# Kernel tuning notes

Hardware: AMD Instinct MI355X
Metric: run time of the kernel (lower is better)

Reference implementation:

```python
import jax, jax.numpy as jnp
import numpy as np
import math

B, T, E, H = 8, 2048, 1024, 64  # batch, seq (== BLOCK_SIZE), emb_size, head_size


def setup_inputs() -> dict:
    key = jax.random.key(0)
    kx, kq, kk, kv = jax.random.split(key, 4)
    s = 1.0 / math.sqrt(E)
    return {
        "x": jax.random.normal(kx, (B, T, E), dtype=jnp.float32),
        "Wq": jax.random.uniform(kq, (H, E), dtype=jnp.float32, minval=-s, maxval=s),
        "Wk": jax.random.uniform(kk, (H, E), dtype=jnp.float32, minval=-s, maxval=s),
        "Wv": jax.random.uniform(kv, (H, E), dtype=jnp.float32, minval=-s, maxval=s),
        "should_mask": 1,
    }


def reference(x, Wq, Wk, Wv, should_mask):
    # Linear(E, H, bias=False): y = x @ W.T
    q = jnp.einsum("bte,he->bth", x, Wq)
    k = jnp.einsum("bte,he->bth", x, Wk)
    v = jnp.einsum("bte,he->bth", x, Wv)
    # NOTE: source multiplies by sqrt(head_size) (not the usual divide)
    affinity = jnp.einsum("bth,bsh->bts", q, k) * jnp.float32(math.sqrt(H))
    if should_mask:
        tril = jnp.tril(jnp.ones((T, T), dtype=bool))
        affinity = jnp.where(tril, affinity, jnp.float32(-jnp.inf))
    weight = jax.nn.softmax(affinity, axis=-1)
    # dropout omitted (eval mode) for determinism
    out = jnp.einsum("bts,bsh->bth", weight, v)
    return out
```

## Files before the change

### kernel.cpp

```cpp
#include <hip/hip_runtime.h>
#include <math.h>

#define NB 8
#define NT 2048
#define NE 1024
#define NH 64

typedef __attribute__((ext_vector_type(8))) short bh8;
typedef __attribute__((ext_vector_type(4))) float f4;

typedef unsigned short u16;

__device__ __forceinline__ u16 bf16rn(float f) {
    unsigned u = __float_as_uint(f);
    u += 0x7FFFu + ((u >> 16) & 1u);
    return (u16)(u >> 16);
}
__device__ __forceinline__ float bf16f(u16 h) {
    return __uint_as_float(((unsigned)h) << 16);
}

__global__ void wprep(const float* __restrict__ wq, const float* __restrict__ wk,
                      const float* __restrict__ wv,
                      u16* __restrict__ whi, u16* __restrict__ wlo)
{
    const int row = blockIdx.x;
    const int k0  = threadIdx.x * 4;
    const float* src = (row < 64)  ? (wq + (size_t)row * NE)
                     : (row < 128) ? (wk + (size_t)(row - 64) * NE)
                     :               (wv + (size_t)(row - 128) * NE);
    float4 v = *(const float4*)(src + k0);
    ushort4 h, l;
    h.x = bf16rn(v.x); l.x = bf16rn(v.x - bf16f(h.x));
    h.y = bf16rn(v.y); l.y = bf16rn(v.y - bf16f(h.y));
    h.z = bf16rn(v.z); l.z = bf16rn(v.z - bf16f(h.z));
    h.w = bf16rn(v.w); l.w = bf16rn(v.w - bf16f(h.w));
    *(ushort4*)(whi + (size_t)row * NE + k0) = h;
    *(ushort4*)(wlo + (size_t)row * NE + k0) = l;
}

__global__ __launch_bounds__(256, 2) void qkv_mfma(
    const float* __restrict__ x, const u16* __restrict__ whi_, const u16* __restrict__ wlo_,
    u16* __restrict__ qhi, u16* __restrict__ qlo,
    u16* __restrict__ khi, u16* __restrict__ klo, u16* __restrict__ vtp)
{
    __shared__ u16 xh[32][72], xl[32][72];
    __shared__ u16 wh[192][72], wl[192][72];

    const int tid  = threadIdx.x;
    const int wid  = tid >> 6;
    const int lane = tid & 63;
    const int t15  = lane & 15, t4 = lane >> 4;
    const int row0 = blockIdx.x * 32;

    const f4 fzero = {0.f, 0.f, 0.f, 0.f};
    f4 acc[2][3];
#pragma unroll
    for (int m = 0; m < 2; ++m)
#pragma unroll
        for (int n = 0; n < 3; ++n) acc[m][n] = fzero;

    for (int kt = 0; kt < NE; kt += 64) {
        __syncthreads();
#pragma unroll
        for (int it = 0; it < 2; ++it) {
            const int f = tid + it * 256;
            const int r = f >> 4, sg = f & 15;
            float4 v = *(const float4*)(x + (size_t)(row0 + r) * NE + kt + sg * 4);
            ushort4 h, l;
            h.x = bf16rn(v.x); l.x = bf16rn(v.x - bf16f(h.x));
            h.y = bf16rn(v.y); l.y = bf16rn(v.y - bf16f(h.y));
            h.z = bf16rn(v.z); l.z = bf16rn(v.z - bf16f(h.z));
            h.w = bf16rn(v.w); l.w = bf16rn(v.w - bf16f(h.w));
            *(ushort4*)&xh[r][sg * 4] = h;
            *(ushort4*)&xl[r][sg * 4] = l;
        }
#pragma unroll
        for (int it = 0; it < 6; ++it) {
            const int f = tid + it * 256;
            const int r = f >> 3, sg = f & 7;
            *(uint4*)&wh[r][sg * 8] = *(const uint4*)(whi_ + (size_t)r * NE + kt + sg * 8);
            *(uint4*)&wl[r][sg * 8] = *(const uint4*)(wlo_ + (size_t)r * NE + kt + sg * 8);
        }
        __syncthreads();

#pragma unroll
        for (int ks = 0; ks < 2; ++ks) {
            bh8 ah[2], al[2];
#pragma unroll
            for (int m = 0; m < 2; ++m) {
                ah[m] = *(const bh8*)&xh[m * 16 + t15][ks * 32 + t4 * 8];
                al[m] = *(const bh8*)&xl[m * 16 + t15][ks * 32 + t4 * 8];
            }
#pragma unroll
            for (int n = 0; n < 3; ++n) {
                const int c = wid * 48 + n * 16 + t15;
                bh8 bhv = *(const bh8*)&wh[c][ks * 32 + t4 * 8];
                bh8 blv = *(const bh8*)&wl[c][ks * 32 + t4 * 8];
#pragma unroll
                for (int m = 0; m < 2; ++m) {
                    acc[m][n] = __builtin_amdgcn_mfma_f32_16x16x32_bf16(ah[m], bhv, acc[m][n], 0, 0, 0);
                    acc[m][n] = __builtin_amdgcn_mfma_f32_16x16x32_bf16(ah[m], blv, acc[m][n], 0, 0, 0);
                    acc[m][n] = __builtin_amdgcn_mfma_f32_16x16x32_bf16(al[m], bhv, acc[m][n], 0, 0, 0);
                }
            }
        }
    }

#pragma unroll
    for (int m = 0; m < 2; ++m) {
#pragma unroll
        for (int n = 0; n < 3; ++n) {
            const int col = wid * 48 + n * 16 + t15;
#pragma unroll
            for (int r = 0; r < 4; ++r) {
                const int row = row0 + m * 16 + t4 * 4 + r;
                float v = acc[m][n][r];
                if (col < 64) {
                    v *= 8.0f;
                    const u16 h = bf16rn(v);
                    qhi[(size_t)row * NH + col] = h;
                    qlo[(size_t)row * NH + col] = bf16rn(v - bf16f(h));
                } else if (col < 128) {
                    const u16 h = bf16rn(v);
                    khi[(size_t)row * NH + (col - 64)] = h;
                    klo[(size_t)row * NH + (col - 64)] = bf16rn(v - bf16f(h));
                } else {
                    const int b   = row >> 11;
                    const int tok = row & (NT - 1);
                    const int c   = tok & 63;
                    const int tp  = (tok & ~63) | ((c & 15) * 4 + (c >> 4));
                    vtp[((size_t)b * NH + (col - 128)) * NT + tp] = bf16rn(v);
                }
            }
        }
    }
}

__global__ __launch_bounds__(256, 2) void attn_mfma(
    const u16* __restrict__ qhi, const u16* __restrict__ qlo,
    const u16* __restrict__ khi, const u16* __restrict__ klo,
    const u16* __restrict__ vtp, const int* __restrict__ smp,
    float* __restrict__ out,
    float* __restrict__ po, float* __restrict__ pm, float* __restrict__ pl)
{
    __shared__ u16 kh[64][72], kl[64][72], vt[64][72], ps[64][72];

    const int tid  = threadIdx.x;
    const int wid  = tid >> 6;
    const int lane = tid & 63;
    const int t15  = lane & 15, t4 = lane >> 4;
    const int b    = blockIdx.y;
    const int u    = 79 - (int)blockIdx.x;
    int qt, c;
    if (u < 8)       { qt = u;                   c = 0; }
    else if (u < 24) { qt = 8  + ((u - 8) >> 1); c = (u - 8) & 1; }
    else if (u < 48) { qt = 16 + (u - 24) / 3;   c = (u - 24) % 3; }
    else             { qt = 24 + ((u - 48) >> 2); c = (u - 48) & 3; }
    const int nch   = (qt + 8) >> 3;
    const int sm    = smp[0];
    const int total = sm ? (qt + 1) : (NT / 64);
    const int jt0   = c * total / nch;
    const int jt1   = (c + 1) * total / nch;
    const int qs    = qt * 64;

    const size_t bb = (size_t)b * NT;

    bh8 qh[2], ql[2];
#pragma unroll
    for (int ks = 0; ks < 2; ++ks) {
        const size_t off = (bb + qs + wid * 16 + t15) * NH + ks * 32 + t4 * 8;
        qh[ks] = *(const bh8*)(qhi + off);
        ql[ks] = *(const bh8*)(qlo + off);
    }

    const f4 fzero = {0.f, 0.f, 0.f, 0.f};
    f4 o[4];
    float m_i[4], l_i[4];
#pragma unroll
    for (int i = 0; i < 4; ++i) { o[i] = fzero; m_i[i] = -INFINITY; l_i[i] = 0.f; }

    for (int jt = jt0; jt < jt1; ++jt) {
        const int js = jt * 64;
        __syncthreads();
#pragma unroll
        for (int it = 0; it < 2; ++it) {
            const int f = tid + it * 256;
            const int r = f >> 3, sg = f & 7;
            *(uint4*)&kh[r][sg * 8] = *(const uint4*)(khi + (bb + js + r) * NH + sg * 8);
            *(uint4*)&kl[r][sg * 8] = *(const uint4*)(klo + (bb + js + r) * NH + sg * 8);
            *(uint4*)&vt[r][sg * 8] = *(const uint4*)(vtp + ((size_t)b * NH + r) * NT + js + sg * 8);
        }
        __syncthreads();

        f4 s[4];
#pragma unroll
        for (int n = 0; n < 4; ++n) s[n] = fzero;
#pragma unroll
        for (int n = 0; n < 4; ++n) {
#pragma unroll
            for (int ks = 0; ks < 2; ++ks) {
                bh8 bhv = *(const bh8*)&kh[n * 16 + t15][ks * 32 + t4 * 8];
                bh8 blv = *(const bh8*)&kl[n * 16 + t15][ks * 32 + t4 * 8];
                s[n] = __builtin_amdgcn_mfma_f32_16x16x32_bf16(qh[ks], bhv, s[n], 0, 0, 0);
                s[n] = __builtin_amdgcn_mfma_f32_16x16x32_bf16(qh[ks], blv, s[n], 0, 0, 0);
                s[n] = __builtin_amdgcn_mfma_f32_16x16x32_bf16(ql[ks], bhv, s[n], 0, 0, 0);
            }
        }

        if (sm && jt == qt) {
#pragma unroll
            for (int n = 0; n < 4; ++n) {
                const int col = n * 16 + t15;
#pragma unroll
                for (int r = 0; r < 4; ++r)
                    if (col > wid * 16 + t4 * 4 + r) s[n][r] = -INFINITY;
            }
        }

#pragma unroll
        for (int r = 0; r < 4; ++r) {
            float rm = fmaxf(fmaxf(s[0][r], s[1][r]), fmaxf(s[2][r], s[3][r]));
            rm = fmaxf(rm, __shfl_xor(rm, 1));
            rm = fmaxf(rm, __shfl_xor(rm, 2));
            rm = fmaxf(rm, __shfl_xor(rm, 4));
            rm = fmaxf(rm, __shfl_xor(rm, 8));
            const float mn = fmaxf(m_i[r], rm);
            const float cf = __expf(m_i[r] - mn);
            const float p0 = __expf(s[0][r] - mn);
            const float p1 = __expf(s[1][r] - mn);
            const float p2 = __expf(s[2][r] - mn);
            const float p3 = __expf(s[3][r] - mn);
            float rs = p0 + p1 + p2 + p3;
            rs += __shfl_xor(rs, 1);
            rs += __shfl_xor(rs, 2);
            rs += __shfl_xor(rs, 4);
            rs += __shfl_xor(rs, 8);
            l_i[r] = l_i[r] * cf + rs;
            m_i[r] = mn;
#pragma unroll
            for (int hs = 0; hs < 4; ++hs) o[hs][r] *= cf;
            ushort4 pw;
            pw.x = bf16rn(p0); pw.y = bf16rn(p1); pw.z = bf16rn(p2); pw.w = bf16rn(p3);
            *(ushort4*)&ps[wid * 16 + t4 * 4 + r][t15 * 4] = pw;
        }

#pragma unroll
        for (int ks = 0; ks < 2; ++ks) {
            bh8 pa = *(const bh8*)&ps[wid * 16 + t15][ks * 32 + t4 * 8];
#pragma unroll
            for (int hs = 0; hs < 4; ++hs) {
                bh8 bv = *(const bh8*)&vt[hs * 16 + t15][ks * 32 + t4 * 8];
                o[hs] = __builtin_amdgcn_mfma_f32_16x16x32_bf16(pa, bv, o[hs], 0, 0, 0);
            }
        }
    }

    if (nch == 1) {
#pragma unroll
        for (int r = 0; r < 4; ++r) {
            const float inv = 1.0f / l_i[r];
            const size_t rowoff = (bb + qs + wid * 16 + t4 * 4 + r) * NH;
#pragma unroll
            for (int hs = 0; hs < 4; ++hs)
                out[rowoff + hs * 16 + t15] = o[hs][r] * inv;
        }
    } else {
        const int slot = (b * 24 + (qt - 8)) * 4 + c;
        float* pop = po + (size_t)slot * 64 * 64;
#pragma unroll
        for (int r = 0; r < 4; ++r) {
            const int rl = wid * 16 + t4 * 4 + r;
#pragma unroll
            for (int hs = 0; hs < 4; ++hs)
                pop[(size_t)rl * 64 + hs * 16 + t15] = o[hs][r];
            if (t15 == 0) {
                pm[(size_t)slot * 64 + rl] = m_i[r];
                pl[(size_t)slot * 64 + rl] = l_i[r];
            }
        }
    }
}

__global__ void attn_combine(const float* __restrict__ po, const float* __restrict__ pm,
                             const float* __restrict__ pl, float* __restrict__ out)
{
    const int qt  = 8 + (int)blockIdx.x;
    const int b   = blockIdx.y;
    const int nch = (qt + 8) >> 3;
    const int tid = threadIdx.x;
    const int r   = tid >> 2;
    const int h0  = (tid & 3) * 16;
    const int base = (b * 24 + (qt - 8)) * 4;

    float m[4], w[4];
    float M = -INFINITY;
#pragma unroll
    for (int cc = 0; cc < 4; ++cc) {
        m[cc] = (cc < nch) ? pm[(size_t)(base + cc) * 64 + r] : -INFINITY;
        M = fmaxf(M, m[cc]);
    }
    float denom = 0.f;
#pragma unroll
    for (int cc = 0; cc < 4; ++cc) {
        w[cc] = (cc < nch) ? __expf(m[cc] - M) : 0.f;
        denom += ((cc < nch) ? pl[(size_t)(base + cc) * 64 + r] : 0.f) * w[cc];
    }
    const float inv = 1.0f / denom;

    const size_t orow = ((size_t)b * NT + (size_t)qt * 64 + r) * NH;
#pragma unroll
    for (int v = 0; v < 4; ++v) {
        float4 acc = make_float4(0.f, 0.f, 0.f, 0.f);
#pragma unroll
        for (int cc = 0; cc < 4; ++cc) {
            if (cc < nch) {
                float4 pv = *(const float4*)(po + ((size_t)(base + cc) * 64 + r) * 64 + h0 + v * 4);
                acc.x += pv.x * w[cc]; acc.y += pv.y * w[cc];
                acc.z += pv.z * w[cc]; acc.w += pv.w * w[cc];
            }
        }
        acc.x *= inv; acc.y *= inv; acc.z *= inv; acc.w *= inv;
        *(float4*)(out + orow + h0 + v * 4) = acc;
    }
}

extern "C" void kernel_launch(void* const* d_in, const int* in_sizes, int n_in,
                              void* d_out, int out_size, void* d_ws, size_t ws_size,
                              hipStream_t stream)
{
    const float* x  = (const float*)d_in[0];
    const float* wq = (const float*)d_in[1];
    const float* wk = (const float*)d_in[2];
    const float* wv = (const float*)d_in[3];
    const int*   sm = (const int*)d_in[4];
    float* out = (float*)d_out;

    u16* whi = (u16*)d_ws;
    u16* wlo = whi + (size_t)192 * NE;
    u16* qhi = wlo + (size_t)192 * NE;
    u16* qlo = qhi + (size_t)NB * NT * NH;
    u16* khi = qlo + (size_t)NB * NT * NH;
    u16* klo = khi + (size_t)NB * NT * NH;
    u16* vtp = klo + (size_t)NB * NT * NH;
    float* po = (float*)(vtp + (size_t)NB * NT * NH);
    float* pm = po + (size_t)NB * 24 * 4 * 64 * 64;
    float* pl = pm + (size_t)NB * 24 * 4 * 64;

    wprep<<<dim3(192), 256, 0, stream>>>(wq, wk, wv, whi, wlo);
    qkv_mfma<<<dim3((NB * NT) / 32), 256, 0, stream>>>(x, whi, wlo, qhi, qlo, khi, klo, vtp);
    attn_mfma<<<dim3(80, NB), 256, 0, stream>>>(qhi, qlo, khi, klo, vtp, sm, out, po, pm, pl);
    attn_combine<<<dim3(24, NB), 256, 0, stream>>>(po, pm, pl, out);
}
```

Baseline: 168.4 us.

## Stage weights via direct global-to-LDS loads with swizzle; load x straight to registers

The weight-prep kernel now writes the bf16 hi/lo weights pre-tiled per 64-wide K slice with an XOR swizzle. The QKV projection copies each slice into unpadded LDS with global_load_lds (16 bytes per lane) and reads it with the matching swizzle to avoid bank conflicts. Each lane now loads x directly into registers in MFMA fragment order and splits it into bf16 hi/lo there, which removes the x LDS buffers and one staging pass. Launch bounds rise to 3 blocks per CU for the projection and 4 for attention, which may force register spills in exchange for occupancy.

```diff
diff --git a/kernel.cpp b/kernel.cpp
--- a/kernel.cpp
+++ b/kernel.cpp
@@ -18,6 +18,14 @@
 }
 __device__ __forceinline__ float bf16f(u16 h) {
     return __uint_as_float(((unsigned)h) << 16);
+}
+__device__ __forceinline__ int swzq(int quad, int row) {
+    return ((quad ^ (row & 7)) << 3);
+}
+__device__ __forceinline__ void gll16(const u16* g, u16* l) {
+    __builtin_amdgcn_global_load_lds(
+        (const __attribute__((address_space(1))) unsigned int*)g,
+        (__attribute__((address_space(3))) unsigned int*)l, 16, 0, 0);
 }
 
 __global__ void wprep(const float* __restrict__ wq, const float* __restrict__ wk,
@@ -35,17 +43,19 @@
     h.y = bf16rn(v.y); l.y = bf16rn(v.y - bf16f(h.y));
     h.z = bf16rn(v.z); l.z = bf16rn(v.z - bf16f(h.z));
     h.w = bf16rn(v.w); l.w = bf16rn(v.w - bf16f(h.w));
-    *(ushort4*)(whi + (size_t)row * NE + k0) = h;
-    *(ushort4*)(wlo + (size_t)row * NE + k0) = l;
-}
-
-__global__ __launch_bounds__(256, 2) void qkv_mfma(
+    const int kt  = k0 >> 6;
+    const int kk  = k0 & 63;
+    const size_t pos = (size_t)kt * (192 * 64) + row * 64 + swzq(kk >> 3, row) + (kk & 7);
+    *(ushort4*)(whi + pos) = h;
+    *(ushort4*)(wlo + pos) = l;
+}
+
+__global__ __launch_bounds__(256, 3) void qkv_mfma(
     const float* __restrict__ x, const u16* __restrict__ whi_, const u16* __restrict__ wlo_,
     u16* __restrict__ qhi, u16* __restrict__ qlo,
     u16* __restrict__ khi, u16* __restrict__ klo, u16* __restrict__ vtp)
 {
-    __shared__ u16 xh[32][72], xl[32][72];
-    __shared__ u16 wh[192][72], wl[192][72];
+    __shared__ u16 wh[192][64], wl[192][64];
 
     const int tid  = threadIdx.x;
     const int wid  = tid >> 6;
@@ -60,43 +70,53 @@
 #pragma unroll
         for (int n = 0; n < 3; ++n) acc[m][n] = fzero;
 
-    for (int kt = 0; kt < NE; kt += 64) {
+    for (int t = 0; t < 16; ++t) {
+        const int kt = t * 64;
+        float4 xr[2][2][2];
+#pragma unroll
+        for (int ks = 0; ks < 2; ++ks)
+#pragma unroll
+            for (int m = 0; m < 2; ++m) {
+                const float* ap = x + (size_t)(row0 + m * 16 + t15) * NE + kt + ks * 32 + t4 * 8;
+                xr[ks][m][0] = *(const float4*)(ap);
+                xr[ks][m][1] = *(const float4*)(ap + 4);
+            }
+
         __syncthreads();
-#pragma unroll
-        for (int it = 0; it < 2; ++it) {
-            const int f = tid + it * 256;
-            const int r = f >> 4, sg = f & 15;
-            float4 v = *(const float4*)(x + (size_t)(row0 + r) * NE + kt + sg * 4);
-            ushort4 h, l;
-            h.x = bf16rn(v.x); l.x = bf16rn(v.x - bf16f(h.x));
-            h.y = bf16rn(v.y); l.y = bf16rn(v.y - bf16f(h.y));
-            h.z = bf16rn(v.z); l.z = bf16rn(v.z - bf16f(h.z));
-            h.w = bf16rn(v.w); l.w = bf16rn(v.w - bf16f(h.w));
-            *(ushort4*)&xh[r][sg * 4] = h;
-            *(ushort4*)&xl[r][sg * 4] = l;
-        }
-#pragma unroll
-        for (int it = 0; it < 6; ++it) {
-            const int f = tid + it * 256;
-            const int r = f >> 3, sg = f & 7;
-            *(uint4*)&wh[r][sg * 8] = *(const uint4*)(whi_ + (size_t)r * NE + kt + sg * 8);
-            *(uint4*)&wl[r][sg * 8] = *(const uint4*)(wlo_ + (size_t)r * NE + kt + sg * 8);
+        {
+            const u16* gh = whi_ + (size_t)t * 12288;
+            const u16* gl = wlo_ + (size_t)t * 12288;
+#pragma unroll
+            for (int it = 0; it < 6; ++it) {
+                const int o = (tid + it * 256) * 8;
+                const int ub = (wid * 64 + it * 256) * 8;
+                gll16(gh + o, &wh[0][0] + ub);
+                gll16(gl + o, &wl[0][0] + ub);
+            }
         }
         __syncthreads();
 
 #pragma unroll
         for (int ks = 0; ks < 2; ++ks) {
+            const int quad = 4 * ks + t4;
             bh8 ah[2], al[2];
 #pragma unroll
             for (int m = 0; m < 2; ++m) {
-                ah[m] = *(const bh8*)&xh[m * 16 + t15][ks * 32 + t4 * 8];
-                al[m] = *(const bh8*)&xl[m * 16 + t15][ks * 32 + t4 * 8];
+                float f8[8];
+                *(float4*)&f8[0] = xr[ks][m][0];
+                *(float4*)&f8[4] = xr[ks][m][1];
+#pragma unroll
+                for (int j = 0; j < 8; ++j) {
+                    const u16 h = bf16rn(f8[j]);
+                    ah[m][j] = (short)h;
+                    al[m][j] = (short)bf16rn(f8[j] - bf16f(h));
+                }
             }
 #pragma unroll
             for (int n = 0; n < 3; ++n) {
                 const int c = wid * 48 + n * 16 + t15;
-                bh8 bhv = *(const bh8*)&wh[c][ks * 32 + t4 * 8];
-                bh8 blv = *(const bh8*)&wl[c][ks * 32 + t4 * 8];
+                bh8 bhv = *(const bh8*)&wh[c][swzq(quad, c)];
+                bh8 blv = *(const bh8*)&wl[c][swzq(quad, c)];
 #pragma unroll
                 for (int m = 0; m < 2; ++m) {
                     acc[m][n] = __builtin_amdgcn_mfma_f32_16x16x32_bf16(ah[m], bhv, acc[m][n], 0, 0, 0);
@@ -122,22 +142,24 @@
                     qhi[(size_t)row * NH + col] = h;
                     qlo[(size_t)row * NH + col] = bf16rn(v - bf16f(h));
                 } else if (col < 128) {
+                    const int cc = col - 64;
                     const u16 h = bf16rn(v);
-                    khi[(size_t)row * NH + (col - 64)] = h;
-                    klo[(size_t)row * NH + (col - 64)] = bf16rn(v - bf16f(h));
+                    khi[(size_t)row * NH + cc] = h;
+                    klo[(size_t)row * NH + cc] = bf16rn(v - bf16f(h));
                 } else {
+                    const int hh  = col - 128;
                     const int b   = row >> 11;
                     const int tok = row & (NT - 1);
-                    const int c   = tok & 63;
-                    const int tp  = (tok & ~63) | ((c & 15) * 4 + (c >> 4));
-                    vtp[((size_t)b * NH + (col - 128)) * NT + tp] = bf16rn(v);
+                    const int cv  = tok & 63;
+                    const int tp  = (tok & ~63) | ((cv & 15) * 4 + (cv >> 4));
+                    vtp[((size_t)b * NH + hh) * NT + tp] = bf16rn(v);
                 }
             }
         }
     }
 }
 
-__global__ __launch_bounds__(256, 2) void attn_mfma(
+__global__ __launch_bounds__(256, 4) void attn_mfma(
     const u16* __restrict__ qhi, const u16* __restrict__ qlo,
     const u16* __restrict__ khi, const u16* __restrict__ klo,
     const u16* __restrict__ vtp, const int* __restrict__ smp,
@@ -200,8 +222,9 @@
         for (int n = 0; n < 4; ++n) {
 #pragma unroll
             for (int ks = 0; ks < 2; ++ks) {
-                bh8 bhv = *(const bh8*)&kh[n * 16 + t15][ks * 32 + t4 * 8];
-                bh8 blv = *(const bh8*)&kl[n * 16 + t15][ks * 32 + t4 * 8];
+                const int rr = n * 16 + t15;
+                bh8 bhv = *(const bh8*)&kh[rr][ks * 32 + t4 * 8];
+                bh8 blv = *(const bh8*)&kl[rr][ks * 32 + t4 * 8];
                 s[n] = __builtin_amdgcn_mfma_f32_16x16x32_bf16(qh[ks], bhv, s[n], 0, 0, 0);
                 s[n] = __builtin_amdgcn_mfma_f32_16x16x32_bf16(qh[ks], blv, s[n], 0, 0, 0);
                 s[n] = __builtin_amdgcn_mfma_f32_16x16x32_bf16(ql[ks], bhv, s[n], 0, 0, 0);
```

Result: slower. 192.4 us (+14.3%).

## Store normalized split-K partial outputs as bf16 and raise attention occupancy target

Applied to the files above, without the earlier changes.

The attention kernel now normalizes each chunk's partial output by its own row sum and writes it as bf16 instead of fp32. The combine kernel is changed to weight each chunk by l*exp(m-M). This halves the partial-output traffic between the attention and combine kernels. Launch bounds are also raised from 2 to 4 blocks per CU, which pushes the compiler to cut registers and may cause spills. Rounding the partials to bf16 adds some output error.

```diff
diff --git a/kernel.cpp b/kernel.cpp
--- a/kernel.cpp
+++ b/kernel.cpp
@@ -137,12 +137,12 @@
     }
 }
 
-__global__ __launch_bounds__(256, 2) void attn_mfma(
+__global__ __launch_bounds__(256, 4) void attn_mfma(
     const u16* __restrict__ qhi, const u16* __restrict__ qlo,
     const u16* __restrict__ khi, const u16* __restrict__ klo,
     const u16* __restrict__ vtp, const int* __restrict__ smp,
     float* __restrict__ out,
-    float* __restrict__ po, float* __restrict__ pm, float* __restrict__ pl)
+    u16* __restrict__ po, float* __restrict__ pm, float* __restrict__ pl)
 {
     __shared__ u16 kh[64][72], kl[64][72], vt[64][72], ps[64][72];
 
@@ -200,8 +200,9 @@
         for (int n = 0; n < 4; ++n) {
 #pragma unroll
             for (int ks = 0; ks < 2; ++ks) {
-                bh8 bhv = *(const bh8*)&kh[n * 16 + t15][ks * 32 + t4 * 8];
-                bh8 blv = *(const bh8*)&kl[n * 16 + t15][ks * 32 + t4 * 8];
+                const int rr = n * 16 + t15;
+                bh8 bhv = *(const bh8*)&kh[rr][ks * 32 + t4 * 8];
+                bh8 blv = *(const bh8*)&kl[rr][ks * 32 + t4 * 8];
                 s[n] = __builtin_amdgcn_mfma_f32_16x16x32_bf16(qh[ks], bhv, s[n], 0, 0, 0);
                 s[n] = __builtin_amdgcn_mfma_f32_16x16x32_bf16(qh[ks], blv, s[n], 0, 0, 0);
                 s[n] = __builtin_amdgcn_mfma_f32_16x16x32_bf16(ql[ks], bhv, s[n], 0, 0, 0);
@@ -267,13 +268,14 @@
         }
     } else {
         const int slot = (b * 24 + (qt - 8)) * 4 + c;
-        float* pop = po + (size_t)slot * 64 * 64;
+        u16* pop = po + (size_t)slot * 64 * 64;
 #pragma unroll
         for (int r = 0; r < 4; ++r) {
             const int rl = wid * 16 + t4 * 4 + r;
+            const float inv = 1.0f / l_i[r];
 #pragma unroll
             for (int hs = 0; hs < 4; ++hs)
-                pop[(size_t)rl * 64 + hs * 16 + t15] = o[hs][r];
+                pop[(size_t)rl * 64 + hs * 16 + t15] = bf16rn(o[hs][r] * inv);
             if (t15 == 0) {
                 pm[(size_t)slot * 64 + rl] = m_i[r];
                 pl[(size_t)slot * 64 + rl] = l_i[r];
@@ -282,7 +284,7 @@
     }
 }
 
-__global__ void attn_combine(const float* __restrict__ po, const float* __restrict__ pm,
+__global__ void attn_combine(const u16* __restrict__ po, const float* __restrict__ pm,
                              const float* __restrict__ pl, float* __restrict__ out)
 {
     const int qt  = 8 + (int)blockIdx.x;
@@ -303,25 +305,30 @@
     float denom = 0.f;
 #pragma unroll
     for (int cc = 0; cc < 4; ++cc) {
-        w[cc] = (cc < nch) ? __expf(m[cc] - M) : 0.f;
-        denom += ((cc < nch) ? pl[(size_t)(base + cc) * 64 + r] : 0.f) * w[cc];
+        w[cc] = (cc < nch) ? pl[(size_t)(base + cc) * 64 + r] * __expf(m[cc] - M) : 0.f;
+        denom += w[cc];
     }
     const float inv = 1.0f / denom;
 
     const size_t orow = ((size_t)b * NT + (size_t)qt * 64 + r) * NH;
 #pragma unroll
-    for (int v = 0; v < 4; ++v) {
-        float4 acc = make_float4(0.f, 0.f, 0.f, 0.f);
+    for (int v = 0; v < 2; ++v) {
+        float acc8[8] = {0.f,0.f,0.f,0.f,0.f,0.f,0.f,0.f};
 #pragma unroll
         for (int cc = 0; cc < 4; ++cc) {
             if (cc < nch) {
-                float4 pv = *(const float4*)(po + ((size_t)(base + cc) * 64 + r) * 64 + h0 + v * 4);
-                acc.x += pv.x * w[cc]; acc.y += pv.y * w[cc];
-                acc.z += pv.z * w[cc]; acc.w += pv.w * w[cc];
-            }
-        }
-        acc.x *= inv; acc.y *= inv; acc.z *= inv; acc.w *= inv;
-        *(float4*)(out + orow + h0 + v * 4) = acc;
+                ushort4 pv = *(const ushort4*)(po + ((size_t)(base + cc) * 64 + r) * 64 + h0 + v * 8);
+                ushort4 pv2 = *(const ushort4*)(po + ((size_t)(base + cc) * 64 + r) * 64 + h0 + v * 8 + 4);
+                acc8[0] += bf16f(pv.x)  * w[cc]; acc8[1] += bf16f(pv.y)  * w[cc];
+                acc8[2] += bf16f(pv.z)  * w[cc]; acc8[3] += bf16f(pv.w)  * w[cc];
+                acc8[4] += bf16f(pv2.x) * w[cc]; acc8[5] += bf16f(pv2.y) * w[cc];
+                acc8[6] += bf16f(pv2.z) * w[cc]; acc8[7] += bf16f(pv2.w) * w[cc];
+            }
+        }
+        float4 o0 = make_float4(acc8[0]*inv, acc8[1]*inv, acc8[2]*inv, acc8[3]*inv);
+        float4 o1 = make_float4(acc8[4]*inv, acc8[5]*inv, acc8[6]*inv, acc8[7]*inv);
+        *(float4*)(out + orow + h0 + v * 8)     = o0;
+        *(float4*)(out + orow + h0 + v * 8 + 4) = o1;
     }
 }
 
@@ -343,8 +350,8 @@
     u16* khi = qlo + (size_t)NB * NT * NH;
     u16* klo = khi + (size_t)NB * NT * NH;
     u16* vtp = klo + (size_t)NB * NT * NH;
-    float* po = (float*)(vtp + (size_t)NB * NT * NH);
-    float* pm = po + (size_t)NB * 24 * 4 * 64 * 64;
+    u16* po  = vtp + (size_t)NB * NT * NH;
+    float* pm = (float*)(po + (size_t)NB * 24 * 4 * 64 * 64);
     float* pl = pm + (size_t)NB * 24 * 4 * 64;
 
     wprep<<<dim3(192), 256, 0, stream>>>(wq, wk, wv, whi, wlo);
```

Result: faster. 160.0 us (-5.0%).
